# Optimization experiments

Hardware: AMD Instinct MI355X
Metric: run time of the kernel (lower is better)

Reference implementation:

```python
import jax, jax.numpy as jnp
import numpy as np

N_NODES = 100000


def gcn_conv(x, edge_index, W, b, n_nodes):
    # PyG GCNConv: add self-loops, symmetric normalization D^-1/2 (A+I) D^-1/2, then XW + b
    xw = x @ W  # [N, out]
    loops = jnp.arange(n_nodes, dtype=edge_index.dtype)
    src = jnp.concatenate([edge_index[0], loops])  # [E+N]
    dst = jnp.concatenate([edge_index[1], loops])
    deg = jax.ops.segment_sum(jnp.ones_like(dst, dtype=xw.dtype), dst, num_segments=n_nodes)
    dinv = jnp.where(deg > 0, deg ** -0.5, 0.0).astype(xw.dtype)
    norm = dinv[src] * dinv[dst]  # [E+N]
    msgs = xw[src] * norm[:, None]  # gather source features, scale
    out = jax.ops.segment_sum(msgs, dst, num_segments=n_nodes)  # scatter-add at dst
    return out + b


def setup_inputs() -> dict:
    key = jax.random.key(0)
    k1, k2, k3, k4 = jax.random.split(key, 4)
    F_in, dim, n_cls, n_edges = 512, 32, 40, 3200000
    x = jax.random.normal(k1, (N_NODES, F_in), dtype=jnp.float32)
    edge_index = jax.random.randint(k2, (2, n_edges), 0, N_NODES, dtype=jnp.int64)
    W1 = jax.random.normal(k3, (F_in, dim), dtype=jnp.float32) * (1.0 / np.sqrt(F_in))
    b1 = jnp.zeros((dim,), dtype=jnp.float32)
    W2 = jax.random.normal(k4, (dim, n_cls), dtype=jnp.float32) * (1.0 / np.sqrt(dim))
    b2 = jnp.zeros((n_cls,), dtype=jnp.float32)
    return {"x": x, "edge_index": edge_index, "W1": W1, "b1": b1, "W2": W2, "b2": b2}


def reference(x, edge_index, W1, b1, W2, b2):
    h = jax.nn.relu(gcn_conv(x, edge_index, W1, b1, N_NODES))
    # F.dropout with training=False (eval) is identity
    logits = gcn_conv(h, edge_index, W2, b2, N_NODES)
    return jax.nn.log_softmax(logits, axis=1)
```

## Files before the change

kernel.cpp:

```cpp
#include <hip/hip_runtime.h>
#include <hip/hip_bf16.h>
#include <math.h>


#define DIM 32
#define NCLS 40
#define F_IN 512
#define BSH 8
#define EPB 8192

__global__ __launch_bounds__(256) void hist_k(const int* __restrict__ dst,
                                              int* __restrict__ gh, int E, int nbk) {
    __shared__ int h[512];
    int tid = threadIdx.x;
    h[tid] = 0; h[tid + 256] = 0;
    __syncthreads();
    int base = blockIdx.x * EPB;
#pragma unroll 4
    for (int k = 0; k < EPB / 256; ++k) {
        int e = base + k * 256 + tid;
        if (e < E) atomicAdd(&h[dst[e] >> BSH], 1);
    }
    __syncthreads();
    if (h[tid]) atomicAdd(&gh[tid], h[tid]);
    if (h[tid + 256]) atomicAdd(&gh[tid + 256], h[tid + 256]);
}

__global__ __launch_bounds__(512) void scanb_k(const int* __restrict__ gh,
                                               int* __restrict__ bbase,
                                               int* __restrict__ gcur, int nbk) {
    __shared__ int sh[512];
    int t = threadIdx.x;
    int c = (t < nbk) ? gh[t] : 0;
    sh[t] = c;
    __syncthreads();
    for (int off = 1; off < 512; off <<= 1) {
        int v = sh[t];
        if (t >= off) v += sh[t - off];
        __syncthreads();
        sh[t] = v;
        __syncthreads();
    }
    int excl = sh[t] - c;
    if (t < nbk) { bbase[t] = excl; gcur[t] = excl; }
    if (t == 0) bbase[nbk] = sh[511];
}

__global__ __launch_bounds__(256) void part_k(const int* __restrict__ src,
                                              const int* __restrict__ dst,
                                              int* __restrict__ gcur,
                                              int2* __restrict__ pairs, int E) {
    __shared__ int2 st[EPB];
    __shared__ int h[512];
    __shared__ int hb[512];
    int tid = threadIdx.x;
    h[tid] = 0; h[tid + 256] = 0;
    __syncthreads();
    int base = blockIdx.x * EPB;
#pragma unroll 4
    for (int k = 0; k < EPB / 256; ++k) {
        int e = base + k * 256 + tid;
        if (e < E) {
            int2 p; p.x = src[e]; p.y = dst[e];
            st[k * 256 + tid] = p;
            atomicAdd(&h[p.y >> BSH], 1);
        }
    }
    __syncthreads();
    for (int b = tid; b < 512; b += 256) {
        int cnt = h[b];
        hb[b] = cnt ? atomicAdd(&gcur[b], cnt) : 0;
        h[b] = 0;
    }
    __syncthreads();
#pragma unroll 4
    for (int k = 0; k < EPB / 256; ++k) {
        int e = base + k * 256 + tid;
        if (e < E) {
            int2 p = st[k * 256 + tid];
            int b = p.y >> BSH;
            int r = atomicAdd(&h[b], 1);
            pairs[hb[b] + r] = p;
        }
    }
}

__global__ __launch_bounds__(256) void build_k(const int2* __restrict__ pairs,
                                               const int* __restrict__ bbase,
                                               int* __restrict__ rowptr,
                                               int* __restrict__ csr,
                                               float* __restrict__ dinv,
                                               int n, int nbk, int E) {
    __shared__ int cnt[256];
    __shared__ int sc[256];
    __shared__ int cur[256];
    int tid = threadIdx.x;
    int b = blockIdx.x;
    int lo = bbase[b], hi = bbase[b + 1];
    cnt[tid] = 0;
    __syncthreads();
    for (int i = lo + tid; i < hi; i += 256)
        atomicAdd(&cnt[pairs[i].y & 255], 1);
    __syncthreads();
    int c = cnt[tid];
    sc[tid] = c;
    __syncthreads();
    for (int off = 1; off < 256; off <<= 1) {
        int v = sc[tid];
        if (tid >= off) v += sc[tid - off];
        __syncthreads();
        sc[tid] = v;
        __syncthreads();
    }
    int excl = sc[tid] - c;
    int v = (b << BSH) + tid;
    if (v < n) {
        rowptr[v] = lo + excl;
        dinv[v] = rsqrtf((float)(c + 1));
    }
    cur[tid] = lo + excl;
    __syncthreads();
    for (int i = lo + tid; i < hi; i += 256) {
        int2 p = pairs[i];
        int pos = atomicAdd(&cur[p.y & 255], 1);
        csr[pos] = p.x;
    }
    if (b == 0 && tid == 0) rowptr[n] = E;
}

#define GBM 64
__global__ __launch_bounds__(256) void gemm1_k(const float* __restrict__ x,
                                               const float* __restrict__ W1,
                                               const float* __restrict__ dinv,
                                               float* __restrict__ xwp, int n) {
    __shared__ float xs[32 * 68];
    __shared__ float ws[32 * 33];
    int tid = threadIdx.x;
    int base = blockIdx.x * GBM;
    int c = tid & 31;
    int rg = tid >> 5;
    float acc[8] = {0.f, 0.f, 0.f, 0.f, 0.f, 0.f, 0.f, 0.f};

    int lr = tid >> 2;
    int lq = tid & 3;
    int grow = base + lr;
    if (grow >= n) grow = n - 1;
    const float* xrow = x + (size_t)grow * F_IN;
    int wk = tid >> 3;
    int wc = tid & 7;

    for (int k0 = 0; k0 < F_IN; k0 += 32) {
        float4 a0 = *(const float4*)(xrow + k0 + lq * 4);
        float4 a1 = *(const float4*)(xrow + k0 + 16 + lq * 4);
        float4 wv = *(const float4*)(W1 + (size_t)(k0 + wk) * DIM + wc * 4);
        __syncthreads();
        xs[(lq * 4 + 0) * 68 + lr] = a0.x;
        xs[(lq * 4 + 1) * 68 + lr] = a0.y;
        xs[(lq * 4 + 2) * 68 + lr] = a0.z;
        xs[(lq * 4 + 3) * 68 + lr] = a0.w;
        xs[(lq * 4 + 16) * 68 + lr] = a1.x;
        xs[(lq * 4 + 17) * 68 + lr] = a1.y;
        xs[(lq * 4 + 18) * 68 + lr] = a1.z;
        xs[(lq * 4 + 19) * 68 + lr] = a1.w;
        ws[wk * 33 + wc * 4 + 0] = wv.x;
        ws[wk * 33 + wc * 4 + 1] = wv.y;
        ws[wk * 33 + wc * 4 + 2] = wv.z;
        ws[wk * 33 + wc * 4 + 3] = wv.w;
        __syncthreads();
#pragma unroll
        for (int kk = 0; kk < 32; ++kk) {
            float w = ws[kk * 33 + c];
            const float4 b0 = *(const float4*)&xs[kk * 68 + rg * 8];
            const float4 b1 = *(const float4*)&xs[kk * 68 + rg * 8 + 4];
            acc[0] += b0.x * w; acc[1] += b0.y * w;
            acc[2] += b0.z * w; acc[3] += b0.w * w;
            acc[4] += b1.x * w; acc[5] += b1.y * w;
            acc[6] += b1.z * w; acc[7] += b1.w * w;
        }
    }
#pragma unroll
    for (int i = 0; i < 8; ++i) {
        int row = base + rg * 8 + i;
        if (row < n) xwp[(size_t)row * DIM + c] = acc[i] * dinv[row];
    }
}

__global__ __launch_bounds__(256) void agg_k(const float* __restrict__ F,
                                             const int* __restrict__ rowptr,
                                             const int* __restrict__ csr,
                                             const float* __restrict__ dinv,
                                             const float* __restrict__ bias,
                                             float* __restrict__ out, int n, int mode) {
    int t = blockIdx.x * 256 + threadIdx.x;
    int v = t >> 3;
    int f4 = t & 7;
    if (v >= n) return;
    const float4* Fv = (const float4*)F;
    float4 s = Fv[(size_t)v * 8 + f4];
    int e = rowptr[v];
    int end = rowptr[v + 1];
    for (; e + 1 < end; e += 2) {
        int u0 = csr[e];
        int u1 = csr[e + 1];
        float4 a = Fv[(size_t)u0 * 8 + f4];
        float4 bq = Fv[(size_t)u1 * 8 + f4];
        s.x += a.x + bq.x; s.y += a.y + bq.y;
        s.z += a.z + bq.z; s.w += a.w + bq.w;
    }
    if (e < end) {
        float4 a = Fv[(size_t)csr[e] * 8 + f4];
        s.x += a.x; s.y += a.y; s.z += a.z; s.w += a.w;
    }
    float dv = dinv[v];
    float4 r;
    if (mode == 1) {
        float4 bb = *(const float4*)(bias + f4 * 4);
        r.x = fmaxf(s.x * dv + bb.x, 0.f) * dv;
        r.y = fmaxf(s.y * dv + bb.y, 0.f) * dv;
        r.z = fmaxf(s.z * dv + bb.z, 0.f) * dv;
        r.w = fmaxf(s.w * dv + bb.w, 0.f) * dv;
    } else {
        r.x = s.x * dv; r.y = s.y * dv; r.z = s.z * dv; r.w = s.w * dv;
    }
    ((float4*)out)[(size_t)v * 8 + f4] = r;
}

__global__ __launch_bounds__(256) void final_k(const float* __restrict__ a2,
                                               const float* __restrict__ W2,
                                               const float* __restrict__ b2,
                                               float* __restrict__ out, int n) {
    __shared__ float w2s[DIM * NCLS];
    __shared__ float b2s[NCLS];
    int tid = threadIdx.x;
    for (int i = tid; i < DIM * NCLS; i += 256) w2s[i] = W2[i];
    if (tid < NCLS) b2s[tid] = b2[tid];
    __syncthreads();
    int lane = tid & 63;
    int wv = tid >> 6;
    int v = blockIdx.x * 4 + wv;
    if (v >= n) return;
    float av = (lane < DIM) ? a2[(size_t)v * DIM + lane] : 0.f;
    float logit = -INFINITY;
    if (lane < NCLS) {
        float accv = b2s[lane];
#pragma unroll
        for (int k = 0; k < DIM; ++k) {
            float a = __shfl(av, k);
            accv += a * w2s[k * NCLS + lane];
        }
        logit = accv;
    }
    float m = logit;
    for (int off = 32; off; off >>= 1) m = fmaxf(m, __shfl_xor(m, off));
    float ex = (lane < NCLS) ? __expf(logit - m) : 0.f;
    float ssum = ex;
    for (int off = 32; off; off >>= 1) ssum += __shfl_xor(ssum, off);
    float lse = m + __logf(ssum);
    if (lane < NCLS) out[(size_t)v * NCLS + lane] = logit - lse;
}

extern "C" void kernel_launch(void* const* d_in, const int* in_sizes, int n_in,
                              void* d_out, int out_size, void* d_ws, size_t ws_size,
                              hipStream_t stream) {
    const float* x  = (const float*)d_in[0];
    const int*   ei = (const int*)d_in[1];
    const float* W1 = (const float*)d_in[2];
    const float* b1 = (const float*)d_in[3];
    const float* W2 = (const float*)d_in[4];
    const float* b2 = (const float*)d_in[5];
    float* out = (float*)d_out;

    int n = in_sizes[0] / F_IN;
    int E = in_sizes[1] / 2;
    const int* src = ei;
    const int* dst = ei + E;
    int nbk = (n + 255) >> BSH;

    char* w = (char*)d_ws;
    size_t off = 0;
    auto alloc = [&](size_t bytes) -> void* {
        void* p = w + off;
        off += (bytes + 255) & ~(size_t)255;
        return p;
    };
    size_t featB = (size_t)n * DIM * 4;
    int*   csr    = (int*)alloc((size_t)E * 4);
    char*  pairsR = (char*)alloc((size_t)E * 8);
    float* a2     = (float*)alloc(featB);
    int*   rowptr = (int*)alloc((size_t)(n + 1) * 4);
    float* dinv   = (float*)alloc((size_t)n * 4);
    int*   gh     = (int*)alloc(512 * 4);
    int*   bbase  = (int*)alloc(513 * 4);
    int*   gcur   = (int*)alloc(512 * 4);
    (void)ws_size;

    int2*  pairs = (int2*)pairsR;
    float* xwp   = (float*)pairsR;
    float* hts   = (float*)(pairsR + featB);

    hipMemsetAsync(gh, 0, 512 * 4, stream);

    int nebk = (E + EPB - 1) / EPB;
    hist_k <<<nebk, 256, 0, stream>>>(dst, gh, E, nbk);
    scanb_k<<<1, 512, 0, stream>>>(gh, bbase, gcur, nbk);
    part_k <<<nebk, 256, 0, stream>>>(src, dst, gcur, pairs, E);
    build_k<<<nbk, 256, 0, stream>>>(pairs, bbase, rowptr, csr, dinv, n, nbk, E);

    gemm1_k<<<(n + GBM - 1) / GBM, 256, 0, stream>>>(x, W1, dinv, xwp, n);
    agg_k<<<((size_t)n * 8 + 255) / 256, 256, 0, stream>>>(xwp, rowptr, csr, dinv, b1, hts, n, 1);
    agg_k<<<((size_t)n * 8 + 255) / 256, 256, 0, stream>>>(hts, rowptr, csr, dinv, nullptr, a2, n, 2);
    final_k<<<(n + 3) / 4, 256, 0, stream>>>(a2, W2, b2, out, n);
}
```

Before: 587.7 us.

## Store intermediate node features in bf16 and fuse second aggregation with output layer

The intermediate feature tables (XW·dinv and the hidden activations) are now stored as packed bf16, which halves the bytes moved by the random neighbor gathers in both aggregation passes. Each thread now handles 8 features through one uint4 load. The second aggregation is fused with the W2 projection and log-softmax through shared memory, so the fp32 a2 buffer and the separate final kernel go away. Accumulation stays in fp32, but the stored features lose precision, which may move results against the fp32 reference.

```diff
diff --git a/kernel.cpp b/kernel.cpp
--- a/kernel.cpp
+++ b/kernel.cpp
@@ -8,6 +8,24 @@
 #define F_IN 512
 #define BSH 8
 #define EPB 8192
+
+__device__ __forceinline__ unsigned int bf16rne(float x) {
+    unsigned int u = __float_as_uint(x);
+    return (u + 0x7fffu + ((u >> 16) & 1u)) >> 16;
+}
+__device__ __forceinline__ unsigned int packpair(float lo, float hi) {
+    return bf16rne(lo) | (bf16rne(hi) << 16);
+}
+__device__ __forceinline__ void unpack8(uint4 u, float* f) {
+    f[0] = __uint_as_float(u.x << 16);
+    f[1] = __uint_as_float(u.x & 0xffff0000u);
+    f[2] = __uint_as_float(u.y << 16);
+    f[3] = __uint_as_float(u.y & 0xffff0000u);
+    f[4] = __uint_as_float(u.z << 16);
+    f[5] = __uint_as_float(u.z & 0xffff0000u);
+    f[6] = __uint_as_float(u.w << 16);
+    f[7] = __uint_as_float(u.w & 0xffff0000u);
+}
 
 __global__ __launch_bounds__(256) void hist_k(const int* __restrict__ dst,
                                               int* __restrict__ gh, int E, int nbk) {
@@ -132,7 +150,7 @@
 __global__ __launch_bounds__(256) void gemm1_k(const float* __restrict__ x,
                                                const float* __restrict__ W1,
                                                const float* __restrict__ dinv,
-                                               float* __restrict__ xwp, int n) {
+                                               unsigned short* __restrict__ xwp, int n) {
     __shared__ float xs[32 * 68];
     __shared__ float ws[32 * 33];
     int tid = threadIdx.x;
@@ -181,82 +199,129 @@
 #pragma unroll
     for (int i = 0; i < 8; ++i) {
         int row = base + rg * 8 + i;
-        if (row < n) xwp[(size_t)row * DIM + c] = acc[i] * dinv[row];
-    }
-}
-
-__global__ __launch_bounds__(256) void agg_k(const float* __restrict__ F,
-                                             const int* __restrict__ rowptr,
-                                             const int* __restrict__ csr,
-                                             const float* __restrict__ dinv,
-                                             const float* __restrict__ bias,
-                                             float* __restrict__ out, int n, int mode) {
+        if (row < n)
+            xwp[(size_t)row * DIM + c] = (unsigned short)bf16rne(acc[i] * dinv[row]);
+    }
+}
+
+__global__ __launch_bounds__(256) void agg1_k(const uint4* __restrict__ F,
+                                              const int* __restrict__ rowptr,
+                                              const int* __restrict__ csr,
+                                              const float* __restrict__ dinv,
+                                              const float* __restrict__ bias,
+                                              uint4* __restrict__ out, int n) {
     int t = blockIdx.x * 256 + threadIdx.x;
-    int v = t >> 3;
-    int f4 = t & 7;
+    int v = t >> 2;
+    int f8 = t & 3;
     if (v >= n) return;
-    const float4* Fv = (const float4*)F;
-    float4 s = Fv[(size_t)v * 8 + f4];
+    float s[8], tmp[8];
+    unpack8(F[(size_t)v * 4 + f8], s);
     int e = rowptr[v];
     int end = rowptr[v + 1];
     for (; e + 1 < end; e += 2) {
         int u0 = csr[e];
         int u1 = csr[e + 1];
-        float4 a = Fv[(size_t)u0 * 8 + f4];
-        float4 bq = Fv[(size_t)u1 * 8 + f4];
-        s.x += a.x + bq.x; s.y += a.y + bq.y;
-        s.z += a.z + bq.z; s.w += a.w + bq.w;
+        uint4 ua = F[(size_t)u0 * 4 + f8];
+        uint4 ub = F[(size_t)u1 * 4 + f8];
+        unpack8(ua, tmp);
+#pragma unroll
+        for (int j = 0; j < 8; ++j) s[j] += tmp[j];
+        unpack8(ub, tmp);
+#pragma unroll
+        for (int j = 0; j < 8; ++j) s[j] += tmp[j];
     }
     if (e < end) {
-        float4 a = Fv[(size_t)csr[e] * 8 + f4];
-        s.x += a.x; s.y += a.y; s.z += a.z; s.w += a.w;
+        unpack8(F[(size_t)csr[e] * 4 + f8], tmp);
+#pragma unroll
+        for (int j = 0; j < 8; ++j) s[j] += tmp[j];
     }
     float dv = dinv[v];
-    float4 r;
-    if (mode == 1) {
-        float4 bb = *(const float4*)(bias + f4 * 4);
-        r.x = fmaxf(s.x * dv + bb.x, 0.f) * dv;
-        r.y = fmaxf(s.y * dv + bb.y, 0.f) * dv;
-        r.z = fmaxf(s.z * dv + bb.z, 0.f) * dv;
-        r.w = fmaxf(s.w * dv + bb.w, 0.f) * dv;
-    } else {
-        r.x = s.x * dv; r.y = s.y * dv; r.z = s.z * dv; r.w = s.w * dv;
-    }
-    ((float4*)out)[(size_t)v * 8 + f4] = r;
-}
-
-__global__ __launch_bounds__(256) void final_k(const float* __restrict__ a2,
-                                               const float* __restrict__ W2,
-                                               const float* __restrict__ b2,
-                                               float* __restrict__ out, int n) {
+    float4 b0 = *(const float4*)(bias + f8 * 8);
+    float4 b1 = *(const float4*)(bias + f8 * 8 + 4);
+    float bb[8] = {b0.x, b0.y, b0.z, b0.w, b1.x, b1.y, b1.z, b1.w};
+    float r[8];
+#pragma unroll
+    for (int j = 0; j < 8; ++j) r[j] = fmaxf(s[j] * dv + bb[j], 0.f) * dv;
+    uint4 o;
+    o.x = packpair(r[0], r[1]);
+    o.y = packpair(r[2], r[3]);
+    o.z = packpair(r[4], r[5]);
+    o.w = packpair(r[6], r[7]);
+    out[(size_t)v * 4 + f8] = o;
+}
+
+__global__ __launch_bounds__(256) void agg2final_k(const uint4* __restrict__ F,
+                                                   const int* __restrict__ rowptr,
+                                                   const int* __restrict__ csr,
+                                                   const float* __restrict__ dinv,
+                                                   const float* __restrict__ W2,
+                                                   const float* __restrict__ b2,
+                                                   float* __restrict__ out, int n) {
     __shared__ float w2s[DIM * NCLS];
     __shared__ float b2s[NCLS];
+    __shared__ float a2s[64 * 33];
     int tid = threadIdx.x;
     for (int i = tid; i < DIM * NCLS; i += 256) w2s[i] = W2[i];
     if (tid < NCLS) b2s[tid] = b2[tid];
-    __syncthreads();
-    int lane = tid & 63;
-    int wv = tid >> 6;
-    int v = blockIdx.x * 4 + wv;
-    if (v >= n) return;
-    float av = (lane < DIM) ? a2[(size_t)v * DIM + lane] : 0.f;
-    float logit = -INFINITY;
-    if (lane < NCLS) {
-        float accv = b2s[lane];
-#pragma unroll
-        for (int k = 0; k < DIM; ++k) {
-            float a = __shfl(av, k);
-            accv += a * w2s[k * NCLS + lane];
-        }
-        logit = accv;
-    }
-    float m = logit;
-    for (int off = 32; off; off >>= 1) m = fmaxf(m, __shfl_xor(m, off));
-    float ex = (lane < NCLS) ? __expf(logit - m) : 0.f;
-    float ssum = ex;
-    for (int off = 32; off; off >>= 1) ssum += __shfl_xor(ssum, off);
+
+    int nl = tid >> 2;
+    int f8 = tid & 3;
+    int v = blockIdx.x * 64 + nl;
+    if (v < n) {
+        float s[8], tmp[8];
+        unpack8(F[(size_t)v * 4 + f8], s);
+        int e = rowptr[v];
+        int end = rowptr[v + 1];
+        for (; e + 1 < end; e += 2) {
+            int u0 = csr[e];
+            int u1 = csr[e + 1];
+            uint4 ua = F[(size_t)u0 * 4 + f8];
+            uint4 ub = F[(size_t)u1 * 4 + f8];
+            unpack8(ua, tmp);
+#pragma unroll
+            for (int j = 0; j < 8; ++j) s[j] += tmp[j];
+            unpack8(ub, tmp);
+#pragma unroll
+            for (int j = 0; j < 8; ++j) s[j] += tmp[j];
+        }
+        if (e < end) {
+            unpack8(F[(size_t)csr[e] * 4 + f8], tmp);
+#pragma unroll
+            for (int j = 0; j < 8; ++j) s[j] += tmp[j];
+        }
+        float dv = dinv[v];
+#pragma unroll
+        for (int j = 0; j < 8; ++j) a2s[nl * 33 + f8 * 8 + j] = s[j] * dv;
+    }
+    __syncthreads();
+
+    int q = f8;
+    float lg[10];
+#pragma unroll
+    for (int c = 0; c < 10; ++c) lg[c] = b2s[q * 10 + c];
+#pragma unroll
+    for (int k = 0; k < DIM; ++k) {
+        float a = a2s[nl * 33 + k];
+        const float* wr = &w2s[k * NCLS + q * 10];
+#pragma unroll
+        for (int c = 0; c < 10; ++c) lg[c] += a * wr[c];
+    }
+    float m = lg[0];
+#pragma unroll
+    for (int c = 1; c < 10; ++c) m = fmaxf(m, lg[c]);
+    m = fmaxf(m, __shfl_xor(m, 1));
+    m = fmaxf(m, __shfl_xor(m, 2));
+    float ssum = 0.f;
+#pragma unroll
+    for (int c = 0; c < 10; ++c) ssum += __expf(lg[c] - m);
+    ssum += __shfl_xor(ssum, 1);
+    ssum += __shfl_xor(ssum, 2);
     float lse = m + __logf(ssum);
-    if (lane < NCLS) out[(size_t)v * NCLS + lane] = logit - lse;
+    if (v < n) {
+        float* o = out + (size_t)v * NCLS + q * 10;
+#pragma unroll
+        for (int c = 0; c < 10; ++c) o[c] = lg[c] - lse;
+    }
 }
 
 extern "C" void kernel_launch(void* const* d_in, const int* in_sizes, int n_in,
@@ -283,10 +348,9 @@
         off += (bytes + 255) & ~(size_t)255;
         return p;
     };
-    size_t featB = (size_t)n * DIM * 4;
+    size_t featB2 = ((size_t)n * DIM * 2 + 255) & ~(size_t)255;
     int*   csr    = (int*)alloc((size_t)E * 4);
     char*  pairsR = (char*)alloc((size_t)E * 8);
-    float* a2     = (float*)alloc(featB);
     int*   rowptr = (int*)alloc((size_t)(n + 1) * 4);
     float* dinv   = (float*)alloc((size_t)n * 4);
     int*   gh     = (int*)alloc(512 * 4);
@@ -294,9 +358,9 @@
     int*   gcur   = (int*)alloc(512 * 4);
     (void)ws_size;
 
-    int2*  pairs = (int2*)pairsR;
-    float* xwp   = (float*)pairsR;
-    float* hts   = (float*)(pairsR + featB);
+    int2*           pairs = (int2*)pairsR;
+    unsigned short* xwp   = (unsigned short*)pairsR;
+    unsigned short* hts   = (unsigned short*)(pairsR + featB2);
 
     hipMemsetAsync(gh, 0, 512 * 4, stream);
 
@@ -307,7 +371,8 @@
     build_k<<<nbk, 256, 0, stream>>>(pairs, bbase, rowptr, csr, dinv, n, nbk, E);
 
     gemm1_k<<<(n + GBM - 1) / GBM, 256, 0, stream>>>(x, W1, dinv, xwp, n);
-    agg_k<<<((size_t)n * 8 + 255) / 256, 256, 0, stream>>>(xwp, rowptr, csr, dinv, b1, hts, n, 1);
-    agg_k<<<((size_t)n * 8 + 255) / 256, 256, 0, stream>>>(hts, rowptr, csr, dinv, nullptr, a2, n, 2);
-    final_k<<<(n + 3) / 4, 256, 0, stream>>>(a2, W2, b2, out, n);
-}
+    agg1_k<<<((size_t)n * 4 + 255) / 256, 256, 0, stream>>>(
+        (const uint4*)xwp, rowptr, csr, dinv, b1, (uint4*)hts, n);
+    agg2final_k<<<(n + 63) / 64, 256, 0, stream>>>(
+        (const uint4*)hts, rowptr, csr, dinv, W2, b2, out, n);
+}
```

New measurement: 532.3 us. 9.4% less time.
